# Performance work log

Hardware: AMD Instinct MI355X
Metric: run time of the kernel (lower is better)

Reference implementation:

```python
import jax, jax.numpy as jnp
import numpy as np

N_ENTITIES = 4096
FEATURE_DIM = 512
CELLS = 39
PAIRS = 8192


def setup_inputs() -> dict:
    key = jax.random.key(0)
    k_emb, k_idx, k_wg, k_wl = jax.random.split(key, 4)
    embedding = jax.random.normal(k_emb, (N_ENTITIES, FEATURE_DIM), dtype=jnp.float32)
    index = jax.random.randint(k_idx, (CELLS, PAIRS, 2), 0, N_ENTITIES, dtype=jnp.int32)
    # kaiming_uniform-style scale for the global bilinear weight
    bound_g = np.sqrt(6.0 / FEATURE_DIM)
    weights_global = jax.random.uniform(k_wg, (FEATURE_DIM, FEATURE_DIM), minval=-bound_g, maxval=bound_g, dtype=jnp.float32)
    # per-cell diagonal scaling vectors (original stores them as [d,1] params)
    weights_local = jax.random.uniform(k_wl, (CELLS, FEATURE_DIM), minval=-bound_g, maxval=bound_g, dtype=jnp.float32)
    return {"embedding": embedding, "index": index,
            "weights_global": weights_global, "weights_local": weights_local}


def reference(embedding, index, weights_global, weights_local):
    # Original per-cell math: einsum('bn,nm,mj,jk,bk->b', A, diag(wl), W, diag(wl), B)
    # diag(wl) @ ... is just elementwise scaling of the gathered embeddings, so:
    #   out[c,p] = sum_{n,k} (A[c,p,n]*wl[c,n]) * W[n,k] * (B[c,p,k]*wl[c,k])
    wl = weights_local[:, None, :]                      # [C,1,d]
    A = embedding[index[..., 0]] * wl                   # [C,P,d]
    B = embedding[index[..., 1]] * wl                   # [C,P,d]
    return jnp.einsum('cpn,nk,cpk->cp', A, weights_global, B)  # [C,P]
```

## Files before the change

kernel.cpp:

```cpp
#include <hip/hip_runtime.h>
#include <stdint.h>

#define NE 4096
#define FD 512
#define NCELLS 39
#define NPAIRS 8192

typedef __attribute__((ext_vector_type(8))) short short8;
typedef __attribute__((ext_vector_type(8))) unsigned short ushort8;
typedef __attribute__((ext_vector_type(4))) float f32x4;

__device__ __forceinline__ unsigned short f2bf(float f) {
  union { float f; uint32_t u; } v; v.f = f;
  uint32_t u = v.u;
  return (unsigned short)((u + 0x7fffu + ((u >> 16) & 1u)) >> 16);
}
__device__ __forceinline__ float bf2f(unsigned short b) {
  return __uint_as_float(((uint32_t)b) << 16);
}

__device__ __forceinline__ void async16(const void* g, void* l) {
  __builtin_amdgcn_global_load_lds((const __attribute__((address_space(1))) void*)g,
                                   (__attribute__((address_space(3))) void*)l, 16, 0, 0);
}

__global__ __launch_bounds__(256) void conv_e(const float* __restrict__ E,
                                              unsigned short* __restrict__ Ebf) {
  const int i = blockIdx.x * 256 + threadIdx.x;
  const float4 v = ((const float4*)E)[i];
  ushort4 o;
  o.x = f2bf(v.x); o.y = f2bf(v.y); o.z = f2bf(v.z); o.w = f2bf(v.w);
  ((ushort4*)Ebf)[i] = o;
}

__global__ __launch_bounds__(256) void prep_w(const float* __restrict__ W,
                                              const float* __restrict__ wl,
                                              unsigned short* __restrict__ Wt,
                                              int c0) {
  __shared__ float tile[32][33];
  const int ci = blockIdx.z;
  const int tn = blockIdx.x * 32, tk = blockIdx.y * 32;
  const int tx = threadIdx.x & 31, ty = threadIdx.x >> 5;
  const float* wlr = wl + (size_t)(c0 + ci) * FD;
#pragma unroll
  for (int i = 0; i < 4; i++) {
    int n = tn + ty + i * 8;
    tile[ty + i * 8][tx] = W[(size_t)n * FD + tk + tx] * wlr[n];
  }
  __syncthreads();
  unsigned short* dst = Wt + (size_t)ci * FD * FD;
#pragma unroll
  for (int i = 0; i < 4; i++) {
    int kout = tk + ty + i * 8;
    dst[(size_t)kout * FD + tn + tx] = f2bf(tile[tx][ty + i * 8]);
  }
}

__global__ __launch_bounds__(256) void gemm_k(const unsigned short* __restrict__ Ebf,
                                              const unsigned short* __restrict__ Wt,
                                              const float* __restrict__ wl,
                                              unsigned short* __restrict__ U,
                                              int c0) {
  __shared__ unsigned short As[128 * 32];
  __shared__ unsigned short Bs[128 * 32];
  const int t = threadIdx.x;
  const int ci = blockIdx.z;
  const unsigned short* Ag = Ebf + (size_t)blockIdx.x * 128 * FD;
  const unsigned short* Bg = Wt + (size_t)ci * FD * FD + (size_t)blockIdx.y * 128 * FD;

  f32x4 acc[4][4];
#pragma unroll
  for (int i = 0; i < 4; i++)
#pragma unroll
    for (int j = 0; j < 4; j++) acc[i][j] = (f32x4){0.f, 0.f, 0.f, 0.f};

  const int wave = t >> 6, lane = t & 63;
  const int wm = (wave & 1) * 64, wn = (wave >> 1) * 64;
  const int lr = lane & 15, lq = lane >> 4;
  const int idx0 = t, idx1 = 256 + t;
  const int r0 = idx0 >> 2, cb0 = (idx0 & 3) * 8;
  const int r1 = idx1 >> 2, cb1 = (idx1 & 3) * 8;

  for (int k0 = 0; k0 < FD; k0 += 32) {
    async16(Ag + (size_t)r0 * FD + k0 + cb0, &As[idx0 * 8]);
    async16(Ag + (size_t)r1 * FD + k0 + cb1, &As[idx1 * 8]);
    async16(Bg + (size_t)r0 * FD + k0 + cb0, &Bs[idx0 * 8]);
    async16(Bg + (size_t)r1 * FD + k0 + cb1, &Bs[idx1 * 8]);
    __syncthreads();
    short8 af[4], bq[4];
#pragma unroll
    for (int mi = 0; mi < 4; mi++) af[mi] = *(const short8*)&As[(wm + mi * 16 + lr) * 32 + lq * 8];
#pragma unroll
    for (int ni = 0; ni < 4; ni++) bq[ni] = *(const short8*)&Bs[(wn + ni * 16 + lr) * 32 + lq * 8];
#pragma unroll
    for (int mi = 0; mi < 4; mi++)
#pragma unroll
      for (int ni = 0; ni < 4; ni++)
        acc[mi][ni] = __builtin_amdgcn_mfma_f32_16x16x32_bf16(af[mi], bq[ni], acc[mi][ni], 0, 0, 0);
    __syncthreads();
  }

  const float* wlr = wl + (size_t)(c0 + ci) * FD;
  unsigned short* Up = U + (size_t)ci * NE * FD;
  float wlv[4];
#pragma unroll
  for (int ni = 0; ni < 4; ni++) wlv[ni] = wlr[blockIdx.y * 128 + wn + ni * 16 + lr];
#pragma unroll
  for (int mi = 0; mi < 4; mi++) {
    int mbase = blockIdx.x * 128 + wm + mi * 16 + lq * 4;
#pragma unroll
    for (int ni = 0; ni < 4; ni++) {
      int n = blockIdx.y * 128 + wn + ni * 16 + lr;
#pragma unroll
      for (int r = 0; r < 4; r++) {
        Up[(size_t)(mbase + r) * FD + n] = f2bf(acc[mi][ni][r] * wlv[ni]);
      }
    }
  }
}

__global__ __launch_bounds__(256) void dot_k(const unsigned short* __restrict__ U,
                                             const unsigned short* __restrict__ Ebf,
                                             const int* __restrict__ index,
                                             float* __restrict__ out,
                                             int c0) {
  const int ci = blockIdx.y;
  const int c = c0 + ci;
  const int wave = threadIdx.x >> 6, lane = threadIdx.x & 63;
  const unsigned short* Uc = U + (size_t)ci * NE * FD;
  const int pbase = blockIdx.x * 32 + wave * 8;
#pragma unroll
  for (int j = 0; j < 8; j++) {
    const int p = pbase + j;
    const int2 id = ((const int2*)index)[(size_t)c * NPAIRS + p];
    const ushort8 uv = *(const ushort8*)(Uc + (size_t)id.x * FD + lane * 8);
    const ushort8 ev = *(const ushort8*)(Ebf + (size_t)id.y * FD + lane * 8);
    float s = 0.f;
#pragma unroll
    for (int q = 0; q < 8; q++) s += bf2f(uv[q]) * bf2f(ev[q]);
#pragma unroll
    for (int off = 32; off > 0; off >>= 1) s += __shfl_down(s, off, 64);
    if (lane == 0) out[(size_t)c * NPAIRS + p] = s;
  }
}

__global__ __launch_bounds__(256) void naive_k(const float* __restrict__ emb,
                                               const int* __restrict__ index,
                                               const float* __restrict__ W,
                                               const float* __restrict__ wl,
                                               float* __restrict__ out) {
  __shared__ float bs[FD];
  __shared__ float red[256];
  const int c = blockIdx.y, p = blockIdx.x;
  const int i0 = index[((size_t)c * NPAIRS + p) * 2];
  const int i1 = index[((size_t)c * NPAIRS + p) * 2 + 1];
  const float* wlc = wl + (size_t)c * FD;
  for (int k = threadIdx.x; k < FD; k += 256) bs[k] = emb[(size_t)i1 * FD + k] * wlc[k];
  __syncthreads();
  float s = 0.f;
  for (int n = threadIdx.x; n < FD; n += 256) {
    const float* wr = W + (size_t)n * FD;
    float tacc = 0.f;
    for (int k = 0; k < FD; k++) tacc += wr[k] * bs[k];
    s += tacc * emb[(size_t)i0 * FD + n] * wlc[n];
  }
  red[threadIdx.x] = s;
  __syncthreads();
  for (int st = 128; st > 0; st >>= 1) {
    if (threadIdx.x < st) red[threadIdx.x] += red[threadIdx.x + st];
    __syncthreads();
  }
  if (threadIdx.x == 0) out[(size_t)c * NPAIRS + p] = red[0];
}

extern "C" void kernel_launch(void* const* d_in, const int* in_sizes, int n_in,
                              void* d_out, int out_size, void* d_ws, size_t ws_size,
                              hipStream_t stream) {
  const float* emb = (const float*)d_in[0];
  const int* index = (const int*)d_in[1];
  const float* Wg = (const float*)d_in[2];
  const float* wl = (const float*)d_in[3];
  float* out = (float*)d_out;

  const size_t ebytes = (size_t)NE * FD * 2;
  const size_t wtcell = (size_t)FD * FD * 2;
  const size_t ucell = (size_t)NE * FD * 2;
  size_t avail = ws_size > ebytes ? ws_size - ebytes : 0;
  int G = (int)(avail / (wtcell + ucell));
  if (G > NCELLS) G = NCELLS;

  if (G < 1) {
    naive_k<<<dim3(NPAIRS, NCELLS), 256, 0, stream>>>(emb, index, Wg, wl, out);
    return;
  }

  unsigned short* Ebf = (unsigned short*)d_ws;
  unsigned short* Wt = (unsigned short*)((char*)d_ws + ebytes);
  unsigned short* U = (unsigned short*)((char*)d_ws + ebytes + (size_t)G * wtcell);

  conv_e<<<dim3((NE * FD / 4) / 256), 256, 0, stream>>>(emb, Ebf);
  for (int c0 = 0; c0 < NCELLS; c0 += G) {
    int g = (NCELLS - c0 < G) ? (NCELLS - c0) : G;
    prep_w<<<dim3(FD / 32, FD / 32, g), 256, 0, stream>>>(Wg, wl, Wt, c0);
    gemm_k<<<dim3(NE / 128, FD / 128, g), 256, 0, stream>>>(Ebf, Wt, wl, U, c0);
    dot_k<<<dim3(NPAIRS / 32, g), 256, 0, stream>>>(U, Ebf, index, out, c0);
  }
}
```

Measured before the change: 245.7 us.

## Chunk the projected dimension so U stays cache-resident and accumulate partial dots

Instead of materializing U per cell group over the full 512-wide output dimension, the output dimension is split into four 128-wide chunks. For each chunk, all 39 cells' U slices are computed and then consumed by a dot kernel that accumulates partial sums into the output. This shrinks the U working set to 39*4096*128 bf16, so the random gathers in dot_k are more likely to hit in the large last-level cache. The dot kernel also processes four pairs per wave, using 16-lane groups. The cost is four extra read-modify-write passes over the output and more kernel launches.

```diff
diff --git a/kernel.cpp b/kernel.cpp
--- a/kernel.cpp
+++ b/kernel.cpp
@@ -5,6 +5,7 @@
 #define FD 512
 #define NCELLS 39
 #define NPAIRS 8192
+#define KC 128
 
 typedef __attribute__((ext_vector_type(8))) short short8;
 typedef __attribute__((ext_vector_type(8))) unsigned short ushort8;
@@ -35,13 +36,12 @@
 
 __global__ __launch_bounds__(256) void prep_w(const float* __restrict__ W,
                                               const float* __restrict__ wl,
-                                              unsigned short* __restrict__ Wt,
-                                              int c0) {
+                                              unsigned short* __restrict__ Wt) {
   __shared__ float tile[32][33];
   const int ci = blockIdx.z;
   const int tn = blockIdx.x * 32, tk = blockIdx.y * 32;
   const int tx = threadIdx.x & 31, ty = threadIdx.x >> 5;
-  const float* wlr = wl + (size_t)(c0 + ci) * FD;
+  const float* wlr = wl + (size_t)ci * FD;
 #pragma unroll
   for (int i = 0; i < 4; i++) {
     int n = tn + ty + i * 8;
@@ -60,13 +60,13 @@
                                               const unsigned short* __restrict__ Wt,
                                               const float* __restrict__ wl,
                                               unsigned short* __restrict__ U,
-                                              int c0) {
+                                              int kc0) {
   __shared__ unsigned short As[128 * 32];
   __shared__ unsigned short Bs[128 * 32];
   const int t = threadIdx.x;
-  const int ci = blockIdx.z;
+  const int ci = blockIdx.y;
   const unsigned short* Ag = Ebf + (size_t)blockIdx.x * 128 * FD;
-  const unsigned short* Bg = Wt + (size_t)ci * FD * FD + (size_t)blockIdx.y * 128 * FD;
+  const unsigned short* Bg = Wt + (size_t)ci * FD * FD + (size_t)kc0 * FD;
 
   f32x4 acc[4][4];
 #pragma unroll
@@ -100,20 +100,20 @@
     __syncthreads();
   }
 
-  const float* wlr = wl + (size_t)(c0 + ci) * FD;
-  unsigned short* Up = U + (size_t)ci * NE * FD;
+  const float* wlr = wl + (size_t)ci * FD + kc0;
+  unsigned short* Up = U + (size_t)ci * NE * KC;
   float wlv[4];
 #pragma unroll
-  for (int ni = 0; ni < 4; ni++) wlv[ni] = wlr[blockIdx.y * 128 + wn + ni * 16 + lr];
+  for (int ni = 0; ni < 4; ni++) wlv[ni] = wlr[wn + ni * 16 + lr];
 #pragma unroll
   for (int mi = 0; mi < 4; mi++) {
     int mbase = blockIdx.x * 128 + wm + mi * 16 + lq * 4;
 #pragma unroll
     for (int ni = 0; ni < 4; ni++) {
-      int n = blockIdx.y * 128 + wn + ni * 16 + lr;
+      int nl = wn + ni * 16 + lr;
 #pragma unroll
       for (int r = 0; r < 4; r++) {
-        Up[(size_t)(mbase + r) * FD + n] = f2bf(acc[mi][ni][r] * wlv[ni]);
+        Up[(size_t)(mbase + r) * KC + nl] = f2bf(acc[mi][ni][r] * wlv[ni]);
       }
     }
   }
@@ -123,24 +123,31 @@
                                              const unsigned short* __restrict__ Ebf,
                                              const int* __restrict__ index,
                                              float* __restrict__ out,
-                                             int c0) {
+                                             int kc0, int first) {
   const int ci = blockIdx.y;
-  const int c = c0 + ci;
   const int wave = threadIdx.x >> 6, lane = threadIdx.x & 63;
-  const unsigned short* Uc = U + (size_t)ci * NE * FD;
-  const int pbase = blockIdx.x * 32 + wave * 8;
-#pragma unroll
-  for (int j = 0; j < 8; j++) {
-    const int p = pbase + j;
-    const int2 id = ((const int2*)index)[(size_t)c * NPAIRS + p];
-    const ushort8 uv = *(const ushort8*)(Uc + (size_t)id.x * FD + lane * 8);
-    const ushort8 ev = *(const ushort8*)(Ebf + (size_t)id.y * FD + lane * 8);
+  const int sub = lane >> 4, l16 = lane & 15;
+  const unsigned short* Uc = U + (size_t)ci * NE * KC;
+  const unsigned short* Ec = Ebf + kc0;
+  const size_t cp = (size_t)ci * NPAIRS;
+  const int pbase = blockIdx.x * 256 + wave * 64 + sub;
+#pragma unroll 4
+  for (int b = 0; b < 16; b++) {
+    const int p = pbase + b * 4;
+    const int2 id = ((const int2*)index)[cp + p];
+    const ushort8 uv = *(const ushort8*)(Uc + (size_t)id.x * KC + l16 * 8);
+    const ushort8 ev = *(const ushort8*)(Ec + (size_t)id.y * FD + l16 * 8);
     float s = 0.f;
 #pragma unroll
     for (int q = 0; q < 8; q++) s += bf2f(uv[q]) * bf2f(ev[q]);
-#pragma unroll
-    for (int off = 32; off > 0; off >>= 1) s += __shfl_down(s, off, 64);
-    if (lane == 0) out[(size_t)c * NPAIRS + p] = s;
+    s += __shfl_xor(s, 8, 64);
+    s += __shfl_xor(s, 4, 64);
+    s += __shfl_xor(s, 2, 64);
+    s += __shfl_xor(s, 1, 64);
+    if (l16 == 0) {
+      float* op = out + cp + p;
+      if (first) *op = s; else *op += s;
+    }
   }
 }
 
@@ -183,26 +190,22 @@
   float* out = (float*)d_out;
 
   const size_t ebytes = (size_t)NE * FD * 2;
-  const size_t wtcell = (size_t)FD * FD * 2;
-  const size_t ucell = (size_t)NE * FD * 2;
-  size_t avail = ws_size > ebytes ? ws_size - ebytes : 0;
-  int G = (int)(avail / (wtcell + ucell));
-  if (G > NCELLS) G = NCELLS;
-
-  if (G < 1) {
+  const size_t wtbytes = (size_t)NCELLS * FD * FD * 2;
+  const size_t ubytes = (size_t)NCELLS * NE * KC * 2;
+  if (ws_size < ebytes + wtbytes + ubytes) {
     naive_k<<<dim3(NPAIRS, NCELLS), 256, 0, stream>>>(emb, index, Wg, wl, out);
     return;
   }
 
   unsigned short* Ebf = (unsigned short*)d_ws;
   unsigned short* Wt = (unsigned short*)((char*)d_ws + ebytes);
-  unsigned short* U = (unsigned short*)((char*)d_ws + ebytes + (size_t)G * wtcell);
+  unsigned short* U = (unsigned short*)((char*)d_ws + ebytes + wtbytes);
 
   conv_e<<<dim3((NE * FD / 4) / 256), 256, 0, stream>>>(emb, Ebf);
-  for (int c0 = 0; c0 < NCELLS; c0 += G) {
-    int g = (NCELLS - c0 < G) ? (NCELLS - c0) : G;
-    prep_w<<<dim3(FD / 32, FD / 32, g), 256, 0, stream>>>(Wg, wl, Wt, c0);
-    gemm_k<<<dim3(NE / 128, FD / 128, g), 256, 0, stream>>>(Ebf, Wt, wl, U, c0);
-    dot_k<<<dim3(NPAIRS / 32, g), 256, 0, stream>>>(U, Ebf, index, out, c0);
-  }
-}
+  prep_w<<<dim3(FD / 32, FD / 32, NCELLS), 256, 0, stream>>>(Wg, wl, Wt);
+  for (int c = 0; c < FD / KC; c++) {
+    const int kc0 = c * KC;
+    gemm_k<<<dim3(NE / 128, NCELLS), 256, 0, stream>>>(Ebf, Wt, wl, U, kc0);
+    dot_k<<<dim3(NPAIRS / 256, NCELLS), 256, 0, stream>>>(U, Ebf, index, out, kc0, c == 0);
+  }
+}
```

After: 279.7 us. 1.14x slower.

## Compute pair dot products with MFMA diagonal and fold wl into W prep

Applied to the files above, without the earlier changes.

Replaces the per-pair wave reduction kernel with one that packs 16 pairs per wave into a 16x16x32 bf16 MFMA chain and reads the diagonal of the result, which removes the shuffle reductions. The right-side local scaling moves from the GEMM epilogue into the transposed-weight preparation. Gathered rows are now read in 64-byte chunks across 16 rows per instruction, which may reduce coalescing. The MFMA also computes 15 wasted off-diagonal dot products for every useful one.

```diff
diff --git a/kernel.cpp b/kernel.cpp
--- a/kernel.cpp
+++ b/kernel.cpp
@@ -14,9 +14,6 @@
   union { float f; uint32_t u; } v; v.f = f;
   uint32_t u = v.u;
   return (unsigned short)((u + 0x7fffu + ((u >> 16) & 1u)) >> 16);
-}
-__device__ __forceinline__ float bf2f(unsigned short b) {
-  return __uint_as_float(((uint32_t)b) << 16);
 }
 
 __device__ __forceinline__ void async16(const void* g, void* l) {
@@ -52,15 +49,13 @@
 #pragma unroll
   for (int i = 0; i < 4; i++) {
     int kout = tk + ty + i * 8;
-    dst[(size_t)kout * FD + tn + tx] = f2bf(tile[tx][ty + i * 8]);
+    dst[(size_t)kout * FD + tn + tx] = f2bf(tile[tx][ty + i * 8] * wlr[kout]);
   }
 }
 
 __global__ __launch_bounds__(256) void gemm_k(const unsigned short* __restrict__ Ebf,
                                               const unsigned short* __restrict__ Wt,
-                                              const float* __restrict__ wl,
-                                              unsigned short* __restrict__ U,
-                                              int c0) {
+                                              unsigned short* __restrict__ U) {
   __shared__ unsigned short As[128 * 32];
   __shared__ unsigned short Bs[128 * 32];
   const int t = threadIdx.x;
@@ -100,11 +95,7 @@
     __syncthreads();
   }
 
-  const float* wlr = wl + (size_t)(c0 + ci) * FD;
   unsigned short* Up = U + (size_t)ci * NE * FD;
-  float wlv[4];
-#pragma unroll
-  for (int ni = 0; ni < 4; ni++) wlv[ni] = wlr[blockIdx.y * 128 + wn + ni * 16 + lr];
 #pragma unroll
   for (int mi = 0; mi < 4; mi++) {
     int mbase = blockIdx.x * 128 + wm + mi * 16 + lq * 4;
@@ -113,35 +104,37 @@
       int n = blockIdx.y * 128 + wn + ni * 16 + lr;
 #pragma unroll
       for (int r = 0; r < 4; r++) {
-        Up[(size_t)(mbase + r) * FD + n] = f2bf(acc[mi][ni][r] * wlv[ni]);
+        Up[(size_t)(mbase + r) * FD + n] = f2bf(acc[mi][ni][r]);
       }
     }
   }
 }
 
-__global__ __launch_bounds__(256) void dot_k(const unsigned short* __restrict__ U,
+__global__ __launch_bounds__(256) void dot_m(const unsigned short* __restrict__ U,
                                              const unsigned short* __restrict__ Ebf,
                                              const int* __restrict__ index,
                                              float* __restrict__ out,
                                              int c0) {
   const int ci = blockIdx.y;
-  const int c = c0 + ci;
+  const int cg = c0 + ci;
   const int wave = threadIdx.x >> 6, lane = threadIdx.x & 63;
-  const unsigned short* Uc = U + (size_t)ci * NE * FD;
-  const int pbase = blockIdx.x * 32 + wave * 8;
-#pragma unroll
-  for (int j = 0; j < 8; j++) {
-    const int p = pbase + j;
-    const int2 id = ((const int2*)index)[(size_t)c * NPAIRS + p];
-    const ushort8 uv = *(const ushort8*)(Uc + (size_t)id.x * FD + lane * 8);
-    const ushort8 ev = *(const ushort8*)(Ebf + (size_t)id.y * FD + lane * 8);
-    float s = 0.f;
-#pragma unroll
-    for (int q = 0; q < 8; q++) s += bf2f(uv[q]) * bf2f(ev[q]);
-#pragma unroll
-    for (int off = 32; off > 0; off >>= 1) s += __shfl_down(s, off, 64);
-    if (lane == 0) out[(size_t)c * NPAIRS + p] = s;
-  }
+  const int m = lane & 15, kg = lane >> 4;
+  const size_t cp = (size_t)cg * NPAIRS;
+  const int jb = (blockIdx.x * 4 + wave) * 16;
+
+  const int2 id = ((const int2*)index)[cp + jb + m];
+  const unsigned short* ar = U + (size_t)ci * NE * FD + (size_t)id.x * FD + kg * 8;
+  const unsigned short* br = Ebf + (size_t)id.y * FD + kg * 8;
+
+  f32x4 acc = (f32x4){0.f, 0.f, 0.f, 0.f};
+#pragma unroll
+  for (int s = 0; s < 16; s++) {
+    const short8 a = *(const short8*)(ar + s * 32);
+    const short8 b = *(const short8*)(br + s * 32);
+    acc = __builtin_amdgcn_mfma_f32_16x16x32_bf16(a, b, acc, 0, 0, 0);
+  }
+  const int r = m - kg * 4;
+  if (r >= 0 && r < 4) out[cp + jb + m] = acc[r];
 }
 
 __global__ __launch_bounds__(256) void naive_k(const float* __restrict__ emb,
@@ -202,7 +195,7 @@
   for (int c0 = 0; c0 < NCELLS; c0 += G) {
     int g = (NCELLS - c0 < G) ? (NCELLS - c0) : G;
     prep_w<<<dim3(FD / 32, FD / 32, g), 256, 0, stream>>>(Wg, wl, Wt, c0);
-    gemm_k<<<dim3(NE / 128, FD / 128, g), 256, 0, stream>>>(Ebf, Wt, wl, U, c0);
-    dot_k<<<dim3(NPAIRS / 32, g), 256, 0, stream>>>(U, Ebf, index, out, c0);
-  }
-}
+    gemm_k<<<dim3(NE / 128, FD / 128, g), 256, 0, stream>>>(Ebf, Wt, U);
+    dot_m<<<dim3(NPAIRS / 64, g), 256, 0, stream>>>(U, Ebf, index, out, c0);
+  }
+}
```

Result: no change. 246.6 us (+0.3%).
